# Kernel tuning notes

Hardware: AMD Instinct MI355X
Metric: run time of the kernel (lower is better)

## Reference

```python
import jax, jax.numpy as jnp
import numpy as np

B, N, D, H = 8, 1024, 512, 512  # batch, nodes/graph, input dim, hidden/output dim
NEG_SLOPE = 0.2


def _gatv2_layer(x, src, dst, Wl, bl, Wr, br, a, bias, nseg):
    """PyG GATv2Conv (heads=1, add_self_loops=False, eval mode -> no dropout).
    message j->i: alpha_ij = softmax_i( a . leaky_relu(xl[j] + xr[i]) ); out[i] = sum_j alpha_ij * xl[j] + bias
    """
    xl = x @ Wl + bl              # [nseg, H] source transform
    xr = x @ Wr + br              # [nseg, H] target transform
    e = jax.nn.leaky_relu(xl[src] + xr[dst], NEG_SLOPE) @ a  # [E] raw scores
    m = jax.lax.stop_gradient(jax.ops.segment_max(e, dst, num_segments=nseg))
    ex = jnp.exp(e - m[dst])
    s = jax.ops.segment_sum(ex, dst, num_segments=nseg)
    alpha = ex / s[dst]                                       # segment softmax over incoming edges
    out = jax.ops.segment_sum(alpha[:, None] * xl[src], dst, num_segments=nseg)
    return out + bias


def setup_inputs() -> dict:
    key = jax.random.key(0)
    rng = np.random.RandomState(0)
    # random per-graph adjacency, avg degree ~16; block-diagonal edge extraction
    adj_np = (rng.rand(B, N, N) < (16.0 / N))
    srcs, dsts = [], []
    for b in range(B):  # matches torch.nonzero(big_adj).t(): row=src, col=dst
        r, c = np.nonzero(adj_np[b])
        srcs.append(r + b * N)
        dsts.append(c + b * N)
    edge_index = jnp.asarray(np.stack([np.concatenate(srcs), np.concatenate(dsts)]).astype(np.int32))

    ks = jax.random.split(key, 32)
    def lin(k, fi, fo):
        return (jax.random.normal(k, (fi, fo), jnp.float32) / np.sqrt(fi)).astype(jnp.float32)
    inp = {
        "batch_graph": jax.random.normal(ks[0], (B, N, D), jnp.float32),
        "adj": jnp.asarray(adj_np.astype(np.float32)),
        "edge_index": edge_index,
    }
    dims = [(D, H), (H, H), (H, H)]
    for i, (fi, fo) in enumerate(dims, start=1):
        k = jax.random.split(ks[i], 6)
        inp[f"Wl{i}"] = lin(k[0], fi, fo)
        inp[f"bl{i}"] = jnp.zeros((fo,), jnp.float32)
        inp[f"Wr{i}"] = lin(k[1], fi, fo)
        inp[f"br{i}"] = jnp.zeros((fo,), jnp.float32)
        inp[f"a{i}"] = (jax.random.normal(k[2], (fo,), jnp.float32) / np.sqrt(fo)).astype(jnp.float32)
        inp[f"bias{i}"] = jnp.zeros((fo,), jnp.float32)
    return inp


def reference(batch_graph, adj, edge_index,
              Wl1, bl1, Wr1, br1, a1, bias1,
              Wl2, bl2, Wr2, br2, a2, bias2,
              Wl3, bl3, Wr3, br3, a3, bias3):
    b, n, d = batch_graph.shape
    nseg = b * n
    x = batch_graph.reshape(nseg, d)
    src, dst = edge_index[0], edge_index[1]
    x = _gatv2_layer(x, src, dst, Wl1, bl1, Wr1, br1, a1, bias1, nseg)  # graph_norm = Identity
    x = _gatv2_layer(x, src, dst, Wl2, bl2, Wr2, br2, a2, bias2, nseg)
    x = _gatv2_layer(x, src, dst, Wl3, bl3, Wr3, br3, a3, bias3, nseg)
    return x.reshape(b, n, -1)
```

## Files before the change

### kernel.cpp

```cpp
#include <hip/hip_runtime.h>
#include <math.h>

#define MTOT 8192
#define HD   512
#define NEG  0.2f

typedef __attribute__((ext_vector_type(8))) short bf16x8;
typedef __attribute__((ext_vector_type(4))) float floatx4;

__device__ inline unsigned short f2bf(float f) {
    unsigned int u = __float_as_uint(f);
    unsigned int r = (u + 0x7FFFu + ((u >> 16) & 1u)) >> 16;
    return (unsigned short)r;
}
__device__ inline float bf2f(unsigned short h) {
    return __uint_as_float(((unsigned int)h) << 16);
}


__global__ void count_deg(const int* __restrict__ dst, int* __restrict__ deg, int E) {
    int i = blockIdx.x * 256 + threadIdx.x;
    if (i < E) atomicAdd(&deg[dst[i]], 1);
}

__global__ __launch_bounds__(1024) void scan_offsets(const int* __restrict__ deg,
                                                     int* __restrict__ offs,
                                                     int* __restrict__ cursor) {
    __shared__ int part[1024];
    int tid = threadIdx.x;
    int base = tid * 8;
    int v[8]; int s = 0;
    #pragma unroll
    for (int i = 0; i < 8; ++i) { v[i] = deg[base + i]; s += v[i]; }
    part[tid] = s;
    __syncthreads();
    for (int off = 1; off < 1024; off <<= 1) {
        int t = (tid >= off) ? part[tid - off] : 0;
        __syncthreads();
        part[tid] += t;
        __syncthreads();
    }
    int run = (tid == 0) ? 0 : part[tid - 1];
    #pragma unroll
    for (int i = 0; i < 8; ++i) {
        offs[base + i] = run;
        cursor[base + i] = run;
        run += v[i];
    }
    if (tid == 1023) offs[MTOT] = run;
}

__global__ void scatter_edges(const int* __restrict__ src, const int* __restrict__ dst,
                              int* __restrict__ cursor, int* __restrict__ csr_src, int E) {
    int i = blockIdx.x * 256 + threadIdx.x;
    if (i < E) {
        int p = atomicAdd(&cursor[dst[i]], 1);
        csr_src[p] = src[i];
    }
}


__global__ __launch_bounds__(256) void prep_convert(
    const float* __restrict__ W0, const float* __restrict__ W1,
    const float* __restrict__ W2, const float* __restrict__ W3,
    const float* __restrict__ W4, const float* __restrict__ W5,
    unsigned short* __restrict__ wtbase,
    const float* __restrict__ X,
    unsigned short* __restrict__ Ahi, unsigned short* __restrict__ Alo)
{
    int z = blockIdx.z;
    if (z == 6) {
        int bid = blockIdx.x * 16 + blockIdx.y;
        int t0 = bid * 256 + threadIdx.x;
        #pragma unroll
        for (int it = 0; it < 16; ++it) {
            int i = (t0 + it * 65536) * 4;
            float4 vv = *(const float4*)(X + i);
            ushort4 h, l;
            h.x = f2bf(vv.x); l.x = f2bf(vv.x - bf2f(h.x));
            h.y = f2bf(vv.y); l.y = f2bf(vv.y - bf2f(h.y));
            h.z = f2bf(vv.z); l.z = f2bf(vv.z - bf2f(h.z));
            h.w = f2bf(vv.w); l.w = f2bf(vv.w - bf2f(h.w));
            *(ushort4*)(Ahi + i) = h;
            *(ushort4*)(Alo + i) = l;
        }
        return;
    }
    const float* W = (z == 0) ? W0 : (z == 1) ? W1 : (z == 2) ? W2
                   : (z == 3) ? W3 : (z == 4) ? W4 : W5;
    int L = z >> 1, lr = z & 1;
    const size_t SZ = (size_t)HD * HD;
    unsigned short* Whi = wtbase + (L * 4 + lr * 2) * SZ;
    unsigned short* Wlo = Whi + SZ;

    __shared__ float t[32][33];
    int bx = blockIdx.x * 32;
    int by = blockIdx.y * 32;
    int tx = threadIdx.x & 31, ty = threadIdx.x >> 5;
    for (int i = ty; i < 32; i += 8)
        t[i][tx] = W[(size_t)(by + i) * HD + bx + tx];
    __syncthreads();
    for (int i = ty; i < 32; i += 8) {
        float vv = t[tx][i];
        unsigned short h = f2bf(vv);
        unsigned short l = f2bf(vv - bf2f(h));
        Whi[(size_t)(bx + i) * HD + by + tx] = h;
        Wlo[(size_t)(bx + i) * HD + by + tx] = l;
    }
}


__global__ __launch_bounds__(256) void gemm_mfma_dual(
    const unsigned short* __restrict__ Ahi, const unsigned short* __restrict__ Alo,
    const unsigned short* __restrict__ Bhi_l, const unsigned short* __restrict__ Blo_l,
    const unsigned short* __restrict__ Bhi_r, const unsigned short* __restrict__ Blo_r,
    const float* __restrict__ bias_l, const float* __restrict__ bias_r,
    float* __restrict__ Cl, float* __restrict__ Cr)
{
    const unsigned short* Bhi = blockIdx.z ? Bhi_r : Bhi_l;
    const unsigned short* Blo = blockIdx.z ? Blo_r : Blo_l;
    const float* bias         = blockIdx.z ? bias_r : bias_l;
    float* C                  = blockIdx.z ? Cr : Cl;

    __shared__ __align__(16) unsigned short lds[4 * 128 * 32];

    int tid = threadIdx.x;
    int wave = tid >> 6, lane = tid & 63;
    int bm = blockIdx.y * 128, bn = blockIdx.x * 128;

    const unsigned short* gsrc[4] = {Ahi, Alo, Bhi, Blo};
    int rowbase[4] = {bm, bm, bn, bn};

    const unsigned short* gbase =
        gsrc[wave] + (size_t)(rowbase[wave] + (lane >> 2)) * 512 + (lane & 3) * 8;

    floatx4 acc[4][4] = {};

    int wm = wave & 1, wn = wave >> 1;
    int lr = lane & 15, lq = lane >> 4;

    for (int k0 = 0; k0 < 512; k0 += 32) {
        const unsigned short* g = gbase + k0;
        #pragma unroll
        for (int rg = 0; rg < 8; ++rg) {
            __builtin_amdgcn_global_load_lds(
                (const __attribute__((address_space(1))) unsigned int*)(g + (size_t)rg * 16 * 512),
                (__attribute__((address_space(3))) unsigned int*)(&lds[wave * 4096 + rg * 512]),
                16, 0, 0);
        }
        __syncthreads();

        bf16x8 ah[4], al[4], bh[4], bl_[4];
        #pragma unroll
        for (int i = 0; i < 4; ++i) {
            int mrow = wm * 64 + i * 16 + lr;
            ah[i]  = *(const bf16x8*)&lds[0 * 4096 + mrow * 32 + lq * 8];
            al[i]  = *(const bf16x8*)&lds[1 * 4096 + mrow * 32 + lq * 8];
            int nrow = wn * 64 + i * 16 + lr;
            bh[i]  = *(const bf16x8*)&lds[2 * 4096 + nrow * 32 + lq * 8];
            bl_[i] = *(const bf16x8*)&lds[3 * 4096 + nrow * 32 + lq * 8];
        }
        #pragma unroll
        for (int i = 0; i < 4; ++i)
            #pragma unroll
            for (int j = 0; j < 4; ++j) {
                acc[i][j] = __builtin_amdgcn_mfma_f32_16x16x32_bf16(ah[i], bh[j],  acc[i][j], 0, 0, 0);
                acc[i][j] = __builtin_amdgcn_mfma_f32_16x16x32_bf16(ah[i], bl_[j], acc[i][j], 0, 0, 0);
                acc[i][j] = __builtin_amdgcn_mfma_f32_16x16x32_bf16(al[i], bh[j],  acc[i][j], 0, 0, 0);
            }
        __syncthreads();
    }

    #pragma unroll
    for (int j = 0; j < 4; ++j) {
        int n = bn + wn * 64 + j * 16 + lr;
        float bv = bias[n];
        #pragma unroll
        for (int i = 0; i < 4; ++i) {
            int mbase = bm + wm * 64 + i * 16 + lq * 4;
            #pragma unroll
            for (int r = 0; r < 4; ++r)
                C[(size_t)(mbase + r) * 512 + n] = acc[i][j][r] + bv;
        }
    }
}


__global__ __launch_bounds__(256) void gat_fused(
    const float* __restrict__ xl, const float* __restrict__ xr,
    const float* __restrict__ avec, const float* __restrict__ bias,
    const int* __restrict__ offs, const int* __restrict__ csr_src,
    float* __restrict__ out, unsigned short* __restrict__ Ohi,
    unsigned short* __restrict__ Olo, int write_fp32)
{
    __shared__ float sc_sh[4][128];
    int gid = blockIdx.x;
    int wv = threadIdx.x >> 6;
    int node = ((gid & 7) << 10) + ((gid >> 3) << 2) + wv;
    int lane = threadIdx.x & 63;

    int beg = offs[node], end = offs[node + 1];
    int deg = end - beg;
    if (deg > 128) deg = 128;

    {
        int sub = lane >> 4, flane = lane & 15;
        float4 av[8], rv[8];
        const float* xrrow = xr + (size_t)node * HD;
        #pragma unroll
        for (int i = 0; i < 8; ++i) {
            av[i] = *(const float4*)(avec + i * 64 + flane * 4);
            rv[i] = *(const float4*)(xrrow + i * 64 + flane * 4);
        }
        for (int p0 = 0; p0 < deg; p0 += 4) {
            int p = p0 + sub;
            bool valid = p < deg;
            int j = csr_src[beg + (valid ? p : 0)];
            const float* xls = xl + (size_t)j * HD;
            float pe = 0.f;
            #pragma unroll
            for (int i = 0; i < 8; ++i) {
                float4 xv = *(const float4*)(xls + i * 64 + flane * 4);
                float t;
                t = xv.x + rv[i].x; pe += av[i].x * (t > 0.f ? t : NEG * t);
                t = xv.y + rv[i].y; pe += av[i].y * (t > 0.f ? t : NEG * t);
                t = xv.z + rv[i].z; pe += av[i].z * (t > 0.f ? t : NEG * t);
                t = xv.w + rv[i].w; pe += av[i].w * (t > 0.f ? t : NEG * t);
            }
            pe += __shfl_xor(pe, 1, 64);
            pe += __shfl_xor(pe, 2, 64);
            pe += __shfl_xor(pe, 4, 64);
            pe += __shfl_xor(pe, 8, 64);
            if (valid && flane == 0) sc_sh[wv][p] = pe;
        }
    }

    float s0v = (lane < deg) ? sc_sh[wv][lane] : -1e30f;
    float s1v = (lane + 64 < deg) ? sc_sh[wv][lane + 64] : -1e30f;
    float m = fmaxf(s0v, s1v);
    #pragma unroll
    for (int off = 32; off; off >>= 1) m = fmaxf(m, __shfl_xor(m, off, 64));
    float e0 = (lane < deg) ? __expf(s0v - m) : 0.f;
    float e1 = (lane + 64 < deg) ? __expf(s1v - m) : 0.f;
    if (lane < deg) sc_sh[wv][lane] = e0;
    if (lane + 64 < deg) sc_sh[wv][lane + 64] = e1;
    float s = e0 + e1;
    #pragma unroll
    for (int off = 32; off; off >>= 1) s += __shfl_xor(s, off, 64);
    float inv = (s > 0.f) ? 1.f / s : 0.f;

    int h0 = lane << 2;
    float4 acc0 = {0.f, 0.f, 0.f, 0.f}, acc1 = {0.f, 0.f, 0.f, 0.f};
    int p = 0;
    for (; p + 4 <= deg; p += 4) {
        float w0 = sc_sh[wv][p + 0], w1 = sc_sh[wv][p + 1];
        float w2 = sc_sh[wv][p + 2], w3 = sc_sh[wv][p + 3];
        int j0 = csr_src[beg + p + 0], j1 = csr_src[beg + p + 1];
        int j2 = csr_src[beg + p + 2], j3 = csr_src[beg + p + 3];
        const float* q0 = xl + (size_t)j0 * HD;
        const float* q1 = xl + (size_t)j1 * HD;
        const float* q2 = xl + (size_t)j2 * HD;
        const float* q3 = xl + (size_t)j3 * HD;
        float4 x00 = *(const float4*)(q0 + h0), x01 = *(const float4*)(q0 + 256 + h0);
        float4 x10 = *(const float4*)(q1 + h0), x11 = *(const float4*)(q1 + 256 + h0);
        float4 x20 = *(const float4*)(q2 + h0), x21 = *(const float4*)(q2 + 256 + h0);
        float4 x30 = *(const float4*)(q3 + h0), x31 = *(const float4*)(q3 + 256 + h0);
        acc0.x += w0 * x00.x + w1 * x10.x + w2 * x20.x + w3 * x30.x;
        acc0.y += w0 * x00.y + w1 * x10.y + w2 * x20.y + w3 * x30.y;
        acc0.z += w0 * x00.z + w1 * x10.z + w2 * x20.z + w3 * x30.z;
        acc0.w += w0 * x00.w + w1 * x10.w + w2 * x20.w + w3 * x30.w;
        acc1.x += w0 * x01.x + w1 * x11.x + w2 * x21.x + w3 * x31.x;
        acc1.y += w0 * x01.y + w1 * x11.y + w2 * x21.y + w3 * x31.y;
        acc1.z += w0 * x01.z + w1 * x11.z + w2 * x21.z + w3 * x31.z;
        acc1.w += w0 * x01.w + w1 * x11.w + w2 * x21.w + w3 * x31.w;
    }
    for (; p < deg; ++p) {
        float w = sc_sh[wv][p];
        int j = csr_src[beg + p];
        const float* q = xl + (size_t)j * HD;
        float4 x0 = *(const float4*)(q + h0), x1 = *(const float4*)(q + 256 + h0);
        acc0.x += w * x0.x; acc0.y += w * x0.y; acc0.z += w * x0.z; acc0.w += w * x0.w;
        acc1.x += w * x1.x; acc1.y += w * x1.y; acc1.z += w * x1.z; acc1.w += w * x1.w;
    }

    float4 b0 = *(const float4*)(bias + h0);
    float4 b1 = *(const float4*)(bias + 256 + h0);
    float4 o0 = {acc0.x * inv + b0.x, acc0.y * inv + b0.y,
                 acc0.z * inv + b0.z, acc0.w * inv + b0.w};
    float4 o1 = {acc1.x * inv + b1.x, acc1.y * inv + b1.y,
                 acc1.z * inv + b1.z, acc1.w * inv + b1.w};

    if (write_fp32) {
        float* orow = out + (size_t)node * HD;
        *(float4*)(orow + h0) = o0;
        *(float4*)(orow + 256 + h0) = o1;
    } else {
        size_t rb = (size_t)node * HD;
        ushort4 h, lo;
        h.x = f2bf(o0.x); lo.x = f2bf(o0.x - bf2f(h.x));
        h.y = f2bf(o0.y); lo.y = f2bf(o0.y - bf2f(h.y));
        h.z = f2bf(o0.z); lo.z = f2bf(o0.z - bf2f(h.z));
        h.w = f2bf(o0.w); lo.w = f2bf(o0.w - bf2f(h.w));
        *(ushort4*)(Ohi + rb + h0) = h;
        *(ushort4*)(Olo + rb + h0) = lo;
        h.x = f2bf(o1.x); lo.x = f2bf(o1.x - bf2f(h.x));
        h.y = f2bf(o1.y); lo.y = f2bf(o1.y - bf2f(h.y));
        h.z = f2bf(o1.z); lo.z = f2bf(o1.z - bf2f(h.z));
        h.w = f2bf(o1.w); lo.w = f2bf(o1.w - bf2f(h.w));
        *(ushort4*)(Ohi + rb + 256 + h0) = h;
        *(ushort4*)(Olo + rb + 256 + h0) = lo;
    }
}


extern "C" void kernel_launch(void* const* d_in, const int* in_sizes, int n_in,
                              void* d_out, int out_size, void* d_ws, size_t ws_size,
                              hipStream_t stream) {
    const float* x0 = (const float*)d_in[0];
    const int* eidx = (const int*)d_in[2];
    int E = in_sizes[2] / 2;
    const int* esrc = eidx;
    const int* edst = eidx + E;

    const float* Wl[3] = {(const float*)d_in[3],  (const float*)d_in[9],  (const float*)d_in[15]};
    const float* bl[3] = {(const float*)d_in[4],  (const float*)d_in[10], (const float*)d_in[16]};
    const float* Wr[3] = {(const float*)d_in[5],  (const float*)d_in[11], (const float*)d_in[17]};
    const float* br[3] = {(const float*)d_in[6],  (const float*)d_in[12], (const float*)d_in[18]};
    const float* av[3] = {(const float*)d_in[7],  (const float*)d_in[13], (const float*)d_in[19]};
    const float* bs[3] = {(const float*)d_in[8],  (const float*)d_in[14], (const float*)d_in[20]};

    char* w = (char*)d_ws;
    unsigned short* Ahi = (unsigned short*)w; w += (size_t)MTOT * HD * 2;
    unsigned short* Alo = (unsigned short*)w; w += (size_t)MTOT * HD * 2;
    unsigned short* wtbase = (unsigned short*)w; w += 12 * (size_t)HD * HD * 2;
    float* xl = (float*)w; w += (size_t)MTOT * HD * 4;
    float* xr = (float*)w; w += (size_t)MTOT * HD * 4;
    int* deg    = (int*)w;
    int* offs   = deg + MTOT;
    int* cursor = offs + MTOT + 8;
    int* csr    = cursor + MTOT;
    const size_t SZ = (size_t)HD * HD;

    prep_convert<<<dim3(16, 16, 7), 256, 0, stream>>>(
        Wl[0], Wr[0], Wl[1], Wr[1], Wl[2], Wr[2], wtbase, x0, Ahi, Alo);

    hipMemsetAsync(deg, 0, MTOT * sizeof(int), stream);
    count_deg<<<(E + 255) / 256, 256, 0, stream>>>(edst, deg, E);
    scan_offsets<<<1, 1024, 0, stream>>>(deg, offs, cursor);
    scatter_edges<<<(E + 255) / 256, 256, 0, stream>>>(esrc, edst, cursor, csr, E);

    dim3 ggrid(HD / 128, MTOT / 128, 2);
    for (int L = 0; L < 3; ++L) {
        gemm_mfma_dual<<<ggrid, 256, 0, stream>>>(Ahi, Alo,
            wtbase + (L * 4 + 0) * SZ, wtbase + (L * 4 + 1) * SZ,
            wtbase + (L * 4 + 2) * SZ, wtbase + (L * 4 + 3) * SZ,
            bl[L], br[L], xl, xr);
        int last = (L == 2);
        gat_fused<<<MTOT / 4, 256, 0, stream>>>(xl, xr, av[L], bs[L], offs, csr,
                                                last ? (float*)d_out : nullptr,
                                                last ? nullptr : Ahi,
                                                last ? nullptr : Alo,
                                                last);
    }
}
```

Baseline: 362.0 us.

## Rebalance GAT edge work across 8 waves per block and fold deg memset

The fused GAT kernel now uses 512 threads per 4-node block. Score computation is spread across all 8 waves over the combined edge range of the 4 nodes, with xr rows staged in shared memory. Each aggregation wave handles half the feature columns with an 8-deep unrolled gather. The degree memset is folded into the prep kernel as an extra z-slice, removing a separate launch. This adds block-level syncs and per-edge node lookup logic in exchange for better load balance across nodes of uneven degree and more memory-level parallelism.

Result: faster. 350.9 us (-3.1%).

```diff
diff --git a/kernel.cpp b/kernel.cpp
--- a/kernel.cpp
+++ b/kernel.cpp
@@ -66,9 +66,16 @@
     const float* __restrict__ W4, const float* __restrict__ W5,
     unsigned short* __restrict__ wtbase,
     const float* __restrict__ X,
-    unsigned short* __restrict__ Ahi, unsigned short* __restrict__ Alo)
+    unsigned short* __restrict__ Ahi, unsigned short* __restrict__ Alo,
+    int* __restrict__ deg)
 {
     int z = blockIdx.z;
+    if (z == 7) {
+        if (blockIdx.x == 0 && blockIdx.y == 0) {
+            for (int i = threadIdx.x; i < MTOT; i += 256) deg[i] = 0;
+        }
+        return;
+    }
     if (z == 6) {
         int bid = blockIdx.x * 16 + blockIdx.y;
         int t0 = bid * 256 + threadIdx.x;
@@ -186,129 +193,136 @@
 }
 
 
-__global__ __launch_bounds__(256) void gat_fused(
+__global__ __launch_bounds__(512) void gat_fused2(
     const float* __restrict__ xl, const float* __restrict__ xr,
     const float* __restrict__ avec, const float* __restrict__ bias,
     const int* __restrict__ offs, const int* __restrict__ csr_src,
     float* __restrict__ out, unsigned short* __restrict__ Ohi,
     unsigned short* __restrict__ Olo, int write_fp32)
 {
+    __shared__ float xr_sh[4][512];
     __shared__ float sc_sh[4][128];
+    __shared__ float inv_sh[4];
+
     int gid = blockIdx.x;
-    int wv = threadIdx.x >> 6;
-    int node = ((gid & 7) << 10) + ((gid >> 3) << 2) + wv;
-    int lane = threadIdx.x & 63;
-
-    int beg = offs[node], end = offs[node + 1];
-    int deg = end - beg;
-    if (deg > 128) deg = 128;
+    int nbase = ((gid & 7) << 10) + ((gid >> 3) << 2);
+    int tid = threadIdx.x;
+    int wv = tid >> 6, lane = tid & 63;
+
+    int o0 = offs[nbase], o1 = offs[nbase + 1], o2 = offs[nbase + 2];
+    int o3 = offs[nbase + 3], o4 = offs[nbase + 4];
+
+    {
+        int row = tid >> 7, col = tid & 127;
+        *(float4*)&xr_sh[row][col * 4] =
+            *(const float4*)(xr + (size_t)(nbase + row) * HD + col * 4);
+    }
+    __syncthreads();
 
     {
         int sub = lane >> 4, flane = lane & 15;
-        float4 av[8], rv[8];
-        const float* xrrow = xr + (size_t)node * HD;
-        #pragma unroll
-        for (int i = 0; i < 8; ++i) {
+        float4 av[8];
+        #pragma unroll
+        for (int i = 0; i < 8; ++i)
             av[i] = *(const float4*)(avec + i * 64 + flane * 4);
-            rv[i] = *(const float4*)(xrrow + i * 64 + flane * 4);
-        }
-        for (int p0 = 0; p0 < deg; p0 += 4) {
+
+        for (int p0 = o0 + wv * 4; p0 < o4; p0 += 32) {
             int p = p0 + sub;
-            bool valid = p < deg;
-            int j = csr_src[beg + (valid ? p : 0)];
+            bool valid = p < o4;
+            int pc = valid ? p : o0;
+            int nid = (pc >= o1) + (pc >= o2) + (pc >= o3);
+            int nb = (nid == 0) ? o0 : (nid == 1) ? o1 : (nid == 2) ? o2 : o3;
+            int local = pc - nb;
+            int j = csr_src[pc];
             const float* xls = xl + (size_t)j * HD;
             float pe = 0.f;
             #pragma unroll
             for (int i = 0; i < 8; ++i) {
                 float4 xv = *(const float4*)(xls + i * 64 + flane * 4);
+                float4 rv = *(const float4*)&xr_sh[nid][i * 64 + flane * 4];
                 float t;
-                t = xv.x + rv[i].x; pe += av[i].x * (t > 0.f ? t : NEG * t);
-                t = xv.y + rv[i].y; pe += av[i].y * (t > 0.f ? t : NEG * t);
-                t = xv.z + rv[i].z; pe += av[i].z * (t > 0.f ? t : NEG * t);
-                t = xv.w + rv[i].w; pe += av[i].w * (t > 0.f ? t : NEG * t);
+                t = xv.x + rv.x; pe += av[i].x * (t > 0.f ? t : NEG * t);
+                t = xv.y + rv.y; pe += av[i].y * (t > 0.f ? t : NEG * t);
+                t = xv.z + rv.z; pe += av[i].z * (t > 0.f ? t : NEG * t);
+                t = xv.w + rv.w; pe += av[i].w * (t > 0.f ? t : NEG * t);
             }
             pe += __shfl_xor(pe, 1, 64);
             pe += __shfl_xor(pe, 2, 64);
             pe += __shfl_xor(pe, 4, 64);
             pe += __shfl_xor(pe, 8, 64);
-            if (valid && flane == 0) sc_sh[wv][p] = pe;
-        }
-    }
-
-    float s0v = (lane < deg) ? sc_sh[wv][lane] : -1e30f;
-    float s1v = (lane + 64 < deg) ? sc_sh[wv][lane + 64] : -1e30f;
-    float m = fmaxf(s0v, s1v);
-    #pragma unroll
-    for (int off = 32; off; off >>= 1) m = fmaxf(m, __shfl_xor(m, off, 64));
-    float e0 = (lane < deg) ? __expf(s0v - m) : 0.f;
-    float e1 = (lane + 64 < deg) ? __expf(s1v - m) : 0.f;
-    if (lane < deg) sc_sh[wv][lane] = e0;
-    if (lane + 64 < deg) sc_sh[wv][lane + 64] = e1;
-    float s = e0 + e1;
-    #pragma unroll
-    for (int off = 32; off; off >>= 1) s += __shfl_xor(s, off, 64);
-    float inv = (s > 0.f) ? 1.f / s : 0.f;
-
-    int h0 = lane << 2;
-    float4 acc0 = {0.f, 0.f, 0.f, 0.f}, acc1 = {0.f, 0.f, 0.f, 0.f};
+            if (valid && flane == 0 && local < 128) sc_sh[nid][local] = pe;
+        }
+    }
+    __syncthreads();
+
+    if (wv < 4) {
+        int nb  = (wv == 0) ? o0 : (wv == 1) ? o1 : (wv == 2) ? o2 : o3;
+        int ne  = (wv == 0) ? o1 : (wv == 1) ? o2 : (wv == 2) ? o3 : o4;
+        int dg = ne - nb; if (dg > 128) dg = 128;
+        float s0v = (lane < dg) ? sc_sh[wv][lane] : -1e30f;
+        float s1v = (lane + 64 < dg) ? sc_sh[wv][lane + 64] : -1e30f;
+        float m = fmaxf(s0v, s1v);
+        #pragma unroll
+        for (int off = 32; off; off >>= 1) m = fmaxf(m, __shfl_xor(m, off, 64));
+        float e0 = (lane < dg) ? __expf(s0v - m) : 0.f;
+        float e1 = (lane + 64 < dg) ? __expf(s1v - m) : 0.f;
+        if (lane < dg) sc_sh[wv][lane] = e0;
+        if (lane + 64 < dg) sc_sh[wv][lane + 64] = e1;
+        float s = e0 + e1;
+        #pragma unroll
+        for (int off = 32; off; off >>= 1) s += __shfl_xor(s, off, 64);
+        if (lane == 0) inv_sh[wv] = (s > 0.f) ? 1.f / s : 0.f;
+    }
+    __syncthreads();
+
+    int nid = wv & 3, half = wv >> 2;
+    int node = nbase + nid;
+    int nb  = (nid == 0) ? o0 : (nid == 1) ? o1 : (nid == 2) ? o2 : o3;
+    int ne  = (nid == 0) ? o1 : (nid == 1) ? o2 : (nid == 2) ? o3 : o4;
+    int dg = ne - nb; if (dg > 128) dg = 128;
+    int hb = half * 256 + lane * 4;
+
+    float4 acc = {0.f, 0.f, 0.f, 0.f};
     int p = 0;
-    for (; p + 4 <= deg; p += 4) {
-        float w0 = sc_sh[wv][p + 0], w1 = sc_sh[wv][p + 1];
-        float w2 = sc_sh[wv][p + 2], w3 = sc_sh[wv][p + 3];
-        int j0 = csr_src[beg + p + 0], j1 = csr_src[beg + p + 1];
-        int j2 = csr_src[beg + p + 2], j3 = csr_src[beg + p + 3];
-        const float* q0 = xl + (size_t)j0 * HD;
-        const float* q1 = xl + (size_t)j1 * HD;
-        const float* q2 = xl + (size_t)j2 * HD;
-        const float* q3 = xl + (size_t)j3 * HD;
-        float4 x00 = *(const float4*)(q0 + h0), x01 = *(const float4*)(q0 + 256 + h0);
-        float4 x10 = *(const float4*)(q1 + h0), x11 = *(const float4*)(q1 + 256 + h0);
-        float4 x20 = *(const float4*)(q2 + h0), x21 = *(const float4*)(q2 + 256 + h0);
-        float4 x30 = *(const float4*)(q3 + h0), x31 = *(const float4*)(q3 + 256 + h0);
-        acc0.x += w0 * x00.x + w1 * x10.x + w2 * x20.x + w3 * x30.x;
-        acc0.y += w0 * x00.y + w1 * x10.y + w2 * x20.y + w3 * x30.y;
-        acc0.z += w0 * x00.z + w1 * x10.z + w2 * x20.z + w3 * x30.z;
-        acc0.w += w0 * x00.w + w1 * x10.w + w2 * x20.w + w3 * x30.w;
-        acc1.x += w0 * x01.x + w1 * x11.x + w2 * x21.x + w3 * x31.x;
-        acc1.y += w0 * x01.y + w1 * x11.y + w2 * x21.y + w3 * x31.y;
-        acc1.z += w0 * x01.z + w1 * x11.z + w2 * x21.z + w3 * x31.z;
-        acc1.w += w0 * x01.w + w1 * x11.w + w2 * x21.w + w3 * x31.w;
-    }
-    for (; p < deg; ++p) {
-        float w = sc_sh[wv][p];
-        int j = csr_src[beg + p];
-        const float* q = xl + (size_t)j * HD;
-        float4 x0 = *(const float4*)(q + h0), x1 = *(const float4*)(q + 256 + h0);
-        acc0.x += w * x0.x; acc0.y += w * x0.y; acc0.z += w * x0.z; acc0.w += w * x0.w;
-        acc1.x += w * x1.x; acc1.y += w * x1.y; acc1.z += w * x1.z; acc1.w += w * x1.w;
-    }
-
-    float4 b0 = *(const float4*)(bias + h0);
-    float4 b1 = *(const float4*)(bias + 256 + h0);
-    float4 o0 = {acc0.x * inv + b0.x, acc0.y * inv + b0.y,
-                 acc0.z * inv + b0.z, acc0.w * inv + b0.w};
-    float4 o1 = {acc1.x * inv + b1.x, acc1.y * inv + b1.y,
-                 acc1.z * inv + b1.z, acc1.w * inv + b1.w};
+    for (; p + 8 <= dg; p += 8) {
+        float w[8]; const float* q[8];
+        #pragma unroll
+        for (int u = 0; u < 8; ++u) {
+            w[u] = sc_sh[nid][p + u];
+            q[u] = xl + (size_t)csr_src[nb + p + u] * HD + hb;
+        }
+        float4 x[8];
+        #pragma unroll
+        for (int u = 0; u < 8; ++u) x[u] = *(const float4*)q[u];
+        #pragma unroll
+        for (int u = 0; u < 8; ++u) {
+            acc.x += w[u] * x[u].x; acc.y += w[u] * x[u].y;
+            acc.z += w[u] * x[u].z; acc.w += w[u] * x[u].w;
+        }
+    }
+    for (; p < dg; ++p) {
+        float w = sc_sh[nid][p];
+        const float* q = xl + (size_t)csr_src[nb + p] * HD + hb;
+        float4 x = *(const float4*)q;
+        acc.x += w * x.x; acc.y += w * x.y; acc.z += w * x.z; acc.w += w * x.w;
+    }
+
+    float inv = inv_sh[nid];
+    float4 bv = *(const float4*)(bias + hb);
+    float4 o = {acc.x * inv + bv.x, acc.y * inv + bv.y,
+                acc.z * inv + bv.z, acc.w * inv + bv.w};
 
     if (write_fp32) {
-        float* orow = out + (size_t)node * HD;
-        *(float4*)(orow + h0) = o0;
-        *(float4*)(orow + 256 + h0) = o1;
+        *(float4*)(out + (size_t)node * HD + hb) = o;
     } else {
-        size_t rb = (size_t)node * HD;
+        size_t rb = (size_t)node * HD + hb;
         ushort4 h, lo;
-        h.x = f2bf(o0.x); lo.x = f2bf(o0.x - bf2f(h.x));
-        h.y = f2bf(o0.y); lo.y = f2bf(o0.y - bf2f(h.y));
-        h.z = f2bf(o0.z); lo.z = f2bf(o0.z - bf2f(h.z));
-        h.w = f2bf(o0.w); lo.w = f2bf(o0.w - bf2f(h.w));
-        *(ushort4*)(Ohi + rb + h0) = h;
-        *(ushort4*)(Olo + rb + h0) = lo;
-        h.x = f2bf(o1.x); lo.x = f2bf(o1.x - bf2f(h.x));
-        h.y = f2bf(o1.y); lo.y = f2bf(o1.y - bf2f(h.y));
-        h.z = f2bf(o1.z); lo.z = f2bf(o1.z - bf2f(h.z));
-        h.w = f2bf(o1.w); lo.w = f2bf(o1.w - bf2f(h.w));
-        *(ushort4*)(Ohi + rb + 256 + h0) = h;
-        *(ushort4*)(Olo + rb + 256 + h0) = lo;
+        h.x = f2bf(o.x); lo.x = f2bf(o.x - bf2f(h.x));
+        h.y = f2bf(o.y); lo.y = f2bf(o.y - bf2f(h.y));
+        h.z = f2bf(o.z); lo.z = f2bf(o.z - bf2f(h.z));
+        h.w = f2bf(o.w); lo.w = f2bf(o.w - bf2f(h.w));
+        *(ushort4*)(Ohi + rb) = h;
+        *(ushort4*)(Olo + rb) = lo;
     }
 }
 
@@ -341,10 +355,9 @@
     int* csr    = cursor + MTOT;
     const size_t SZ = (size_t)HD * HD;
 
-    prep_convert<<<dim3(16, 16, 7), 256, 0, stream>>>(
-        Wl[0], Wr[0], Wl[1], Wr[1], Wl[2], Wr[2], wtbase, x0, Ahi, Alo);
-
-    hipMemsetAsync(deg, 0, MTOT * sizeof(int), stream);
+    prep_convert<<<dim3(16, 16, 8), 256, 0, stream>>>(
+        Wl[0], Wr[0], Wl[1], Wr[1], Wl[2], Wr[2], wtbase, x0, Ahi, Alo, deg);
+
     count_deg<<<(E + 255) / 256, 256, 0, stream>>>(edst, deg, E);
     scan_offsets<<<1, 1024, 0, stream>>>(deg, offs, cursor);
     scatter_edges<<<(E + 255) / 256, 256, 0, stream>>>(esrc, edst, cursor, csr, E);
@@ -356,10 +369,10 @@
             wtbase + (L * 4 + 2) * SZ, wtbase + (L * 4 + 3) * SZ,
             bl[L], br[L], xl, xr);
         int last = (L == 2);
-        gat_fused<<<MTOT / 4, 256, 0, stream>>>(xl, xr, av[L], bs[L], offs, csr,
-                                                last ? (float*)d_out : nullptr,
-                                                last ? nullptr : Ahi,
-                                                last ? nullptr : Alo,
-                                                last);
-    }
-}
+        gat_fused2<<<MTOT / 4, 512, 0, stream>>>(xl, xr, av[L], bs[L], offs, csr,
+                                                 last ? (float*)d_out : nullptr,
+                                                 last ? nullptr : Ahi,
+                                                 last ? nullptr : Alo,
+                                                 last);
+    }
+}
```
